# Performance work log

Measured on AMD Instinct MI355X. Metric: run time of the kernel, lower is better.

The kernel has to match this reference:

```python
import jax, jax.numpy as jnp
import numpy as np

#   x_out = Dy(alpha) @ J @ Dy(beta) @ J @ Dy(gamma) @ x   (per-irrep block diagonal)
# Dy(theta) is the sparse cos/sin y-rotation (exactly what encode_rotation_angle feeds
# into the segmented tensor product), and J = D(rotation by pi about (x+y)/sqrt(2)) is
# the constant Wigner matrix that conjugates a y-rotation into an x-rotation.

LMAX = 8
MUL = 64
LS = list(range(LMAX + 1))
DIM = MUL * sum(2 * l + 1 for l in LS)  # 5184
BATCH = 16384


def _so3_generators(l):
    # real antisymmetric so(3) generators for degree l (e3nn/cuE convention)
    m = np.arange(-l, l)
    raising = np.diag(-np.sqrt(l * (l + 1) - m * (m + 1)), k=-1).astype(np.complex128)
    m = np.arange(-l + 1, l + 1)
    lowering = np.diag(np.sqrt(l * (l + 1) - m * (m - 1)), k=1).astype(np.complex128)
    m = np.arange(-l, l + 1)
    X = np.stack([0.5 * (raising + lowering), np.diag(1j * m).astype(np.complex128),
                  -0.5j * (raising - lowering)])
    # change of basis complex -> real spherical harmonics
    q = np.zeros((2 * l + 1, 2 * l + 1), dtype=np.complex128)
    for mm in range(-l, 0):
        q[l + mm, l + abs(mm)] = 1.0 / np.sqrt(2)
        q[l + mm, l - abs(mm)] = -1j / np.sqrt(2)
    q[l, l] = 1.0
    for mm in range(1, l + 1):
        q[l + mm, l + abs(mm)] = (-1.0) ** mm / np.sqrt(2)
        q[l + mm, l - abs(mm)] = 1j * (-1.0) ** mm / np.sqrt(2)
    q = (-1j) ** l * q
    X = np.conj(q.T)[None] @ X @ q[None]
    return np.real(X)  # (3, 2l+1, 2l+1)


def _expm(A):
    w, V = np.linalg.eig(A.astype(np.complex128))
    return np.real(V @ np.diag(np.exp(w)) @ np.linalg.inv(V))


_J, _FREQ = [], []
for _l in LS:
    _X = _so3_generators(_l)
    # J = expm(pi * (Xx + Xy)/sqrt(2)): involution with J Dy(b) J = Dx(b)
    _J.append(jnp.asarray(_expm((np.pi / np.sqrt(2.0)) * (_X[0] + _X[1])), dtype=jnp.float32))
    _d = 2 * _l + 1
    # antidiagonal of the y-generator gives the per-row trig frequencies (+/- m)
    _FREQ.append(jnp.asarray(_X[1][np.arange(_d), _d - 1 - np.arange(_d)], dtype=jnp.float32))


def _rot_y(theta, freq, seg):
    # theta: [B], freq: [d], seg: [B, d, mul] (ir_mul layout)
    ang = freq * theta[:, None]                      # [B, d]
    return jnp.cos(ang)[..., None] * seg + jnp.sin(ang)[..., None] * seg[:, ::-1, :]


def setup_inputs() -> dict:
    key = jax.random.key(0)
    kg, kb, ka, kx = jax.random.split(key, 4)
    pi = float(np.pi)
    return {
        "gamma": jax.random.uniform(kg, (BATCH,), jnp.float32, -pi, pi),
        "beta": jax.random.uniform(kb, (BATCH,), jnp.float32, -pi, pi),
        "alpha": jax.random.uniform(ka, (BATCH,), jnp.float32, -pi, pi),
        "x": jax.random.normal(kx, (BATCH, DIM), jnp.float32),
    }


def reference(gamma, beta, alpha, x):
    outs = []
    off = 0
    for l, J, freq in zip(LS, _J, _FREQ):
        d = 2 * l + 1
        seg = x[:, off:off + d * MUL].reshape(-1, d, MUL)  # [B, 2l+1, mul]
        off += d * MUL
        seg = _rot_y(gamma, freq, seg)                      # first rotation about y
        seg = jnp.einsum('ij,bjm->bim', J, seg)
        seg = _rot_y(beta, freq, seg)                       # rotation about x (J-conjugated)
        seg = jnp.einsum('ij,bjm->bim', J, seg)
        seg = _rot_y(alpha, freq, seg)                      # last rotation about y
        outs.append(seg.reshape(-1, d * MUL))
    return jnp.concatenate(outs, axis=1)
```

## Files before the change

### kernel.cpp

```cpp
#include <hip/hip_runtime.h>
#include <math.h>
#include <complex>


#define LMAX 8
#define BATCH 16384
#define DIM 5184

__host__ __device__ constexpr int joff_u(int l) {
    int o = 0;
    for (int k = 0; k < l; ++k) { int dk = 2 * k + 1; o += dk * dk; }
    return o;
}
#define NJ 969

struct JPack { float v[NJ]; };

static void compute_J_host(JPack* jp) {
    for (int l = 0; l <= LMAX; ++l) {
        const int d = 2 * l + 1;
        std::complex<double> q[289], Ac[289], T1[289];
        double A[289], E[289], Tm[289], P[289];
        const double is2 = 1.0 / std::sqrt(2.0);
        static const double pr[4] = {1.0, 0.0, -1.0, 0.0};
        static const double pim[4] = {0.0, -1.0, 0.0, 1.0};
        const int ph = l & 3;
        for (int i = 0; i < d; ++i) {
            for (int j = 0; j < d; ++j) {
                double re = 0.0, im = 0.0;
                const int mm = i - l;
                if (mm < 0) {
                    if (j == l - mm) re = is2;
                    if (j == l + mm) im = -is2;
                } else if (mm == 0) {
                    if (j == l) re = 1.0;
                } else {
                    const double sgn = (mm & 1) ? -1.0 : 1.0;
                    if (j == l + mm) re = sgn * is2;
                    if (j == l - mm) im = sgn * is2;
                }
                q[i * d + j] = std::complex<double>(re * pr[ph] - im * pim[ph],
                                                    re * pim[ph] + im * pr[ph]);
                double xr = 0.0;
                if (j == i - 1) {
                    const double m = (double)(i - 1 - l);
                    xr += -0.5 * std::sqrt((double)l * (l + 1) - m * (m + 1));
                }
                if (j == i + 1) {
                    const double m = (double)(i - l + 1);
                    xr += 0.5 * std::sqrt((double)l * (l + 1) - m * (m - 1));
                }
                Ac[i * d + j] = std::complex<double>(xr, (i == j) ? (double)(i - l) : 0.0);
            }
        }
        for (int i = 0; i < d; ++i)
            for (int j = 0; j < d; ++j) {
                std::complex<double> s = 0.0;
                for (int k = 0; k < d; ++k) s += Ac[i * d + k] * q[k * d + j];
                T1[i * d + j] = s;
            }
        for (int i = 0; i < d; ++i)
            for (int j = 0; j < d; ++j) {
                std::complex<double> s = 0.0;
                for (int k = 0; k < d; ++k) s += std::conj(q[k * d + i]) * T1[k * d + j];
                A[i * d + j] = s.real() * (M_PI / std::sqrt(2.0));
            }
        double mx = 0.0;
        for (int i = 0; i < d; ++i) {
            double s = 0.0;
            for (int k = 0; k < d; ++k) s += std::fabs(A[i * d + k]);
            mx = std::fmax(mx, s);
        }
        int sh = 0;
        while (mx > 0.25 && sh < 60) { mx *= 0.5; ++sh; }
        const double sc = std::ldexp(1.0, -sh);
        for (int t = 0; t < d * d; ++t) A[t] *= sc;
        for (int i = 0; i < d; ++i)
            for (int j = 0; j < d; ++j) E[i * d + j] = Tm[i * d + j] = (i == j) ? 1.0 : 0.0;
        for (int kk = 1; kk <= 16; ++kk) {
            for (int i = 0; i < d; ++i)
                for (int j = 0; j < d; ++j) {
                    double s = 0.0;
                    for (int k = 0; k < d; ++k) s += Tm[i * d + k] * A[k * d + j];
                    P[i * d + j] = s / (double)kk;
                }
            for (int t = 0; t < d * d; ++t) { Tm[t] = P[t]; E[t] += P[t]; }
        }
        for (int q2 = 0; q2 < sh; ++q2) {
            for (int i = 0; i < d; ++i)
                for (int j = 0; j < d; ++j) {
                    double s = 0.0;
                    for (int k = 0; k < d; ++k) s += E[i * d + k] * E[k * d + j];
                    P[i * d + j] = s;
                }
            for (int t = 0; t < d * d; ++t) E[t] = P[t];
        }
        for (int i = 0; i < d; ++i)
            for (int j = 0; j < d; ++j)
                jp->v[joff_u(l) + i * d + j] = (float)E[i * d + j];
    }
}

template <int L>
__device__ __forceinline__ void rotY(float* v, float c1, float s1) {
    if constexpr (L >= 1) {
        float ck = c1, sk = s1;
#pragma unroll
        for (int k = 1; k <= L; ++k) {
            const int i = L - k, r = L + k;
            const float vi = v[i], vr = v[r];
            v[i] = ck * vi + sk * vr;
            v[r] = ck * vr - sk * vi;
            if (k < L) {
                const float cn = ck * c1 - sk * s1;
                const float sn = sk * c1 + ck * s1;
                ck = cn; sk = sn;
            }
        }
    }
}

template <int L>
__device__ __forceinline__ void jmul(float* __restrict__ out, const float* __restrict__ a,
                                     const JPack& jp) {
    constexpr int D = 2 * L + 1;
    constexpr int OFF = joff_u(L);
#pragma unroll
    for (int i = 0; i < D; ++i) {
        float s = 0.f;
#pragma unroll
        for (int j = 0; j < D; ++j) s += jp.v[OFF + i * D + j] * a[j];
        out[i] = s;
    }
}

template <int L>
__device__ __forceinline__ void process(const float* __restrict__ xb, float* __restrict__ ob,
                                        const JPack& jp,
                                        float cg, float sg, float cb, float sb,
                                        float ca, float sa) {
    constexpr int D = 2 * L + 1;
    const float* p = xb + 64 * L * L;
    float A[D], B[D];
#pragma unroll
    for (int i = 0; i < D; ++i) A[i] = p[i * 64];
    rotY<L>(A, cg, sg);
    jmul<L>(B, A, jp);
    rotY<L>(B, cb, sb);
    jmul<L>(A, B, jp);
    rotY<L>(A, ca, sa);
    float* o = ob + 64 * L * L;
#pragma unroll
    for (int i = 0; i < D; ++i) __builtin_nontemporal_store(A[i], o + i * 64);
}

__global__ __launch_bounds__(256) void rot_main(const float* __restrict__ gamma,
                                                const float* __restrict__ beta,
                                                const float* __restrict__ alpha,
                                                const float* __restrict__ x,
                                                float* __restrict__ out,
                                                const JPack jp) {
    const int wave = threadIdx.x >> 6;
    const int lane = threadIdx.x & 63;
    const int b = blockIdx.x * 4 + wave;

    const float gm = gamma[b], bt = beta[b], al = alpha[b];
    float sg, cg, sb, cb, sa, ca;
    __sincosf(gm, &sg, &cg);
    __sincosf(bt, &sb, &cb);
    __sincosf(al, &sa, &ca);

    const float* xb = x + (size_t)b * DIM + lane;
    float* ob = out + (size_t)b * DIM + lane;

    process<0>(xb, ob, jp, cg, sg, cb, sb, ca, sa);
    process<1>(xb, ob, jp, cg, sg, cb, sb, ca, sa);
    process<2>(xb, ob, jp, cg, sg, cb, sb, ca, sa);
    process<3>(xb, ob, jp, cg, sg, cb, sb, ca, sa);
    process<4>(xb, ob, jp, cg, sg, cb, sb, ca, sa);
    process<5>(xb, ob, jp, cg, sg, cb, sb, ca, sa);
    process<6>(xb, ob, jp, cg, sg, cb, sb, ca, sa);
    process<7>(xb, ob, jp, cg, sg, cb, sb, ca, sa);
    process<8>(xb, ob, jp, cg, sg, cb, sb, ca, sa);
}

extern "C" void kernel_launch(void* const* d_in, const int* in_sizes, int n_in,
                              void* d_out, int out_size, void* d_ws, size_t ws_size,
                              hipStream_t stream) {
    const float* gamma = (const float*)d_in[0];
    const float* beta  = (const float*)d_in[1];
    const float* alpha = (const float*)d_in[2];
    const float* x     = (const float*)d_in[3];
    float* out = (float*)d_out;

    JPack jp;
    compute_J_host(&jp);

    hipLaunchKernelGGL(rot_main, dim3(BATCH / 4), dim3(256), 0, stream,
                       gamma, beta, alpha, x, out, jp);
}
```

Baseline: 136.9 us.

## Precompose per-sample Wigner matrices in LDS and apply one matvec per irrep

Instead of applying three sparse y-rotations and two J multiplications per lane, each wavefront first builds the full composed rotation matrix Dy(a)·J·Dy(b)·J·Dy(g) for every degree in shared memory, using a per-sample sin/cos table. Each lane then performs a single dense matvec per irrep, reading padded float4 rows from LDS. This removes the redundant per-channel J products and recurrence work, but adds block-wide __syncthreads, LDS traffic and a composition phase per sample. The host-side J computation is also cached in a static and copied to the workspace each call instead of being recomputed and passed as a kernel argument.

```diff
diff --git a/kernel.cpp b/kernel.cpp
--- a/kernel.cpp
+++ b/kernel.cpp
@@ -6,13 +6,21 @@
 #define LMAX 8
 #define BATCH 16384
 #define DIM 5184
-
+#define NJ 969
+#define NP 1140
+
+__host__ __device__ constexpr int d_of(int l) { return 2 * l + 1; }
 __host__ __device__ constexpr int joff_u(int l) {
     int o = 0;
-    for (int k = 0; k < l; ++k) { int dk = 2 * k + 1; o += dk * dk; }
+    for (int k = 0; k < l; ++k) o += d_of(k) * d_of(k);
     return o;
 }
-#define NJ 969
+__host__ __device__ constexpr int rp_of(int l) { return (d_of(l) + 3) & ~3; }
+__host__ __device__ constexpr int poff_u(int l) {
+    int o = 0;
+    for (int k = 0; k < l; ++k) o += d_of(k) * rp_of(k);
+    return o;
+}
 
 struct JPack { float v[NJ]; };
 
@@ -102,56 +110,67 @@
 }
 
 template <int L>
-__device__ __forceinline__ void rotY(float* v, float c1, float s1) {
-    if constexpr (L >= 1) {
-        float ck = c1, sk = s1;
-#pragma unroll
-        for (int k = 1; k <= L; ++k) {
-            const int i = L - k, r = L + k;
-            const float vi = v[i], vr = v[r];
-            v[i] = ck * vi + sk * vr;
-            v[r] = ck * vr - sk * vi;
-            if (k < L) {
-                const float cn = ck * c1 - sk * s1;
-                const float sn = sk * c1 + ck * s1;
-                ck = cn; sk = sn;
-            }
-        }
-    }
+__device__ __forceinline__ void compose(const float* __restrict__ sJ,
+                                        float* __restrict__ Pw,
+                                        float* __restrict__ Dw,
+                                        const float (&T)[3][2][17],
+                                        int lane) {
+    constexpr int d = d_of(L), h = (d + 1) / 2, RP = rp_of(L);
+    const float* J = sJ + joff_u(L);
+    float* D = Dw + poff_u(L);
+    for (int t = lane; t < h * d; t += 64) {
+        const int i = t / d, j = t - i * d;
+        const int i2 = d - 1 - i, j2 = d - 1 - j;
+        const float cg = T[0][0][(L - j) + 8], sg = T[0][1][(L - j) + 8];
+        const float p1a = J[i * d + j] * cg - J[i * d + j2] * sg;
+        const float p1b = J[i2 * d + j] * cg - J[i2 * d + j2] * sg;
+        const float cb = T[1][0][(L - i) + 8], sb = T[1][1][(L - i) + 8];
+        Pw[i * d + j]  = cb * p1a + sb * p1b;
+        Pw[i2 * d + j] = cb * p1b - sb * p1a;
+    }
+    __syncthreads();
+    for (int t = lane; t < h * d; t += 64) {
+        const int i = t / d, j = t - i * d;
+        const int i2 = d - 1 - i;
+        float ta = 0.f, tb = 0.f;
+#pragma unroll
+        for (int k = 0; k < d; ++k) {
+            const float p = Pw[k * d + j];
+            ta += J[i * d + k] * p;
+            tb += J[i2 * d + k] * p;
+        }
+        const float ca = T[2][0][(L - i) + 8], sa = T[2][1][(L - i) + 8];
+        D[i * RP + j]  = ca * ta + sa * tb;
+        D[i2 * RP + j] = ca * tb - sa * ta;
+    }
+    __syncthreads();
 }
 
 template <int L>
-__device__ __forceinline__ void jmul(float* __restrict__ out, const float* __restrict__ a,
-                                     const JPack& jp) {
-    constexpr int D = 2 * L + 1;
-    constexpr int OFF = joff_u(L);
-#pragma unroll
-    for (int i = 0; i < D; ++i) {
-        float s = 0.f;
-#pragma unroll
-        for (int j = 0; j < D; ++j) s += jp.v[OFF + i * D + j] * a[j];
-        out[i] = s;
-    }
-}
-
-template <int L>
-__device__ __forceinline__ void process(const float* __restrict__ xb, float* __restrict__ ob,
-                                        const JPack& jp,
-                                        float cg, float sg, float cb, float sb,
-                                        float ca, float sa) {
-    constexpr int D = 2 * L + 1;
+__device__ __forceinline__ void apply(const float* __restrict__ xb,
+                                      float* __restrict__ ob,
+                                      const float* __restrict__ Dw) {
+    constexpr int d = d_of(L), RP = rp_of(L);
+    const float* __restrict__ D = Dw + poff_u(L);
     const float* p = xb + 64 * L * L;
-    float A[D], B[D];
-#pragma unroll
-    for (int i = 0; i < D; ++i) A[i] = p[i * 64];
-    rotY<L>(A, cg, sg);
-    jmul<L>(B, A, jp);
-    rotY<L>(B, cb, sb);
-    jmul<L>(A, B, jp);
-    rotY<L>(A, ca, sa);
     float* o = ob + 64 * L * L;
-#pragma unroll
-    for (int i = 0; i < D; ++i) __builtin_nontemporal_store(A[i], o + i * 64);
+    float A[d];
+#pragma unroll
+    for (int i = 0; i < d; ++i) A[i] = p[i * 64];
+#pragma unroll
+    for (int i = 0; i < d; ++i) {
+        const float4* row = reinterpret_cast<const float4*>(D + i * RP);
+        float acc = 0.f;
+#pragma unroll
+        for (int q = 0; q < RP / 4; ++q) {
+            const float4 f = row[q];
+            if (4 * q + 0 < d) acc += f.x * A[4 * q + 0];
+            if (4 * q + 1 < d) acc += f.y * A[4 * q + 1];
+            if (4 * q + 2 < d) acc += f.z * A[4 * q + 2];
+            if (4 * q + 3 < d) acc += f.w * A[4 * q + 3];
+        }
+        __builtin_nontemporal_store(acc, o + i * 64);
+    }
 }
 
 __global__ __launch_bounds__(256) void rot_main(const float* __restrict__ gamma,
@@ -159,29 +178,54 @@
                                                 const float* __restrict__ alpha,
                                                 const float* __restrict__ x,
                                                 float* __restrict__ out,
-                                                const JPack jp) {
-    const int wave = threadIdx.x >> 6;
-    const int lane = threadIdx.x & 63;
+                                                const float* __restrict__ Jg) {
+    __shared__ float sJ[NJ];
+    __shared__ __align__(16) float sD[4][NP];
+    __shared__ float sP[4][289];
+    __shared__ float sT[4][3][2][17];
+
+    const int tid = threadIdx.x;
+    const int wave = tid >> 6, lane = tid & 63;
     const int b = blockIdx.x * 4 + wave;
 
-    const float gm = gamma[b], bt = beta[b], al = alpha[b];
-    float sg, cg, sb, cb, sa, ca;
-    __sincosf(gm, &sg, &cg);
-    __sincosf(bt, &sb, &cb);
-    __sincosf(al, &sa, &ca);
+    for (int i = tid; i < NJ; i += 256) sJ[i] = Jg[i];
+
+    if (lane < 51) {
+        const int a = lane / 17, mm = lane - a * 17;
+        const float th = (a == 0) ? gamma[b] : ((a == 1) ? beta[b] : alpha[b]);
+        float s, c;
+        __sincosf((float)(mm - 8) * th, &s, &c);
+        sT[wave][a][0][mm] = c;
+        sT[wave][a][1][mm] = s;
+    }
+    __syncthreads();
+
+    const float (&T)[3][2][17] = sT[wave];
+    float* Pw = sP[wave];
+    float* Dw = sD[wave];
+
+    compose<0>(sJ, Pw, Dw, T, lane);
+    compose<1>(sJ, Pw, Dw, T, lane);
+    compose<2>(sJ, Pw, Dw, T, lane);
+    compose<3>(sJ, Pw, Dw, T, lane);
+    compose<4>(sJ, Pw, Dw, T, lane);
+    compose<5>(sJ, Pw, Dw, T, lane);
+    compose<6>(sJ, Pw, Dw, T, lane);
+    compose<7>(sJ, Pw, Dw, T, lane);
+    compose<8>(sJ, Pw, Dw, T, lane);
 
     const float* xb = x + (size_t)b * DIM + lane;
     float* ob = out + (size_t)b * DIM + lane;
 
-    process<0>(xb, ob, jp, cg, sg, cb, sb, ca, sa);
-    process<1>(xb, ob, jp, cg, sg, cb, sb, ca, sa);
-    process<2>(xb, ob, jp, cg, sg, cb, sb, ca, sa);
-    process<3>(xb, ob, jp, cg, sg, cb, sb, ca, sa);
-    process<4>(xb, ob, jp, cg, sg, cb, sb, ca, sa);
-    process<5>(xb, ob, jp, cg, sg, cb, sb, ca, sa);
-    process<6>(xb, ob, jp, cg, sg, cb, sb, ca, sa);
-    process<7>(xb, ob, jp, cg, sg, cb, sb, ca, sa);
-    process<8>(xb, ob, jp, cg, sg, cb, sb, ca, sa);
+    apply<0>(xb, ob, Dw);
+    apply<1>(xb, ob, Dw);
+    apply<2>(xb, ob, Dw);
+    apply<3>(xb, ob, Dw);
+    apply<4>(xb, ob, Dw);
+    apply<5>(xb, ob, Dw);
+    apply<6>(xb, ob, Dw);
+    apply<7>(xb, ob, Dw);
+    apply<8>(xb, ob, Dw);
 }
 
 extern "C" void kernel_launch(void* const* d_in, const int* in_sizes, int n_in,
@@ -193,9 +237,12 @@
     const float* x     = (const float*)d_in[3];
     float* out = (float*)d_out;
 
-    JPack jp;
-    compute_J_host(&jp);
+    static JPack jp;
+    static bool init = false;
+    if (!init) { compute_J_host(&jp); init = true; }
+
+    hipMemcpyAsync(d_ws, jp.v, sizeof(JPack), hipMemcpyHostToDevice, stream);
 
     hipLaunchKernelGGL(rot_main, dim3(BATCH / 4), dim3(256), 0, stream,
-                       gamma, beta, alpha, x, out, jp);
-}
+                       gamma, beta, alpha, x, out, (const float*)d_ws);
+}
```

Result: slower. 149.2 us (+9.0%).
